# Kernel tuning notes

Measured on AMD Instinct MI355X. Metric: run time of the kernel, lower is better.

## Reference

```python
import jax, jax.numpy as jnp
import numpy as np

N = 50000      # nodes
E = 1000000    # edges
D = 128        # in_dim
H = 4          # heads
C = 32         # hidden_dim (per head)
ED = 16        # edge_input_dim
NEG_SLOPE = 0.2
LN_EPS = 1e-5


def setup_inputs() -> dict:
    key = jax.random.key(0)
    ks = jax.random.split(key, 8)
    w = lambda k, shape: jax.random.normal(k, shape, jnp.float32) * 0.05
    return {
        "x": jax.random.normal(ks[0], (N, D), jnp.float32),
        "edge_index": jax.random.randint(ks[1], (2, E), 0, N, jnp.int32),
        "edge_attr": jax.random.normal(ks[2], (E, ED), jnp.float32),
        "Wl": w(ks[3], (D, H * C)),          # lin_l weight (source transform)
        "bl": jnp.zeros((H * C,), jnp.float32),
        "Wr": w(ks[4], (D, H * C)),          # lin_r weight (target transform)
        "br": jnp.zeros((H * C,), jnp.float32),
        "We": w(ks[5], (ED, H * C)),         # lin_edge weight (no bias in PyG)
        "att": w(ks[6], (H, C)),             # attention vector a per head
        "bias_out": jnp.zeros((H * C,), jnp.float32),  # conv output bias
        "gamma": jnp.ones((H * C,), jnp.float32),      # LayerNorm weight
        "beta": jnp.zeros((H * C,), jnp.float32),      # LayerNorm bias
    }


def _layer_norm(h, gamma, beta):
    mu = jnp.mean(h, axis=-1, keepdims=True)
    var = jnp.mean(jnp.square(h - mu), axis=-1, keepdims=True)
    return (h - mu) * jax.lax.rsqrt(var + LN_EPS) * gamma + beta


def reference(x, edge_index, edge_attr, Wl, bl, Wr, br, We, att, bias_out, gamma, beta):
    src = edge_index[0]
    dst = edge_index[1]

    # GATv2: separate linear transforms for source (lin_l) and target (lin_r)
    x_l = (x @ Wl + bl).reshape(N, H, C)
    x_r = (x @ Wr + br).reshape(N, H, C)
    e = (edge_attr @ We).reshape(E, H, C)

    # per-edge message: leaky_relu(x_l[src] + x_r[dst] + edge), score = <., att>
    m = jax.nn.leaky_relu(x_l[src] + x_r[dst] + e, NEG_SLOPE)   # [E,H,C]
    alpha = jnp.einsum("ehc,hc->eh", m, att)                      # [E,H]

    # segment softmax over incoming edges of each destination node
    amax = jax.ops.segment_max(alpha, dst, num_segments=N)        # [N,H]
    ex = jnp.exp(alpha - amax[dst])
    denom = jax.ops.segment_sum(ex, dst, num_segments=N)          # [N,H]
    attn = ex / (denom[dst] + 1e-16)                              # [E,H]

    # scatter-aggregate weighted source features (x_j = x_l[src] in GATv2)
    out = jax.ops.segment_sum(attn[:, :, None] * x_l[src], dst, num_segments=N)  # [N,H,C]
    out = out.reshape(N, H * C) + bias_out

    h = jax.nn.elu(out)          # dropout is identity at inference
    return _layer_norm(h + x, gamma, beta)   # residual is Identity (D == H*C)
```

## Files before the change

### kernel.cpp

```cpp
#include <hip/hip_runtime.h>
#include <math.h>

#define NN 50000
#define EE 1000000

#define LINB 782
#define CNT_THREADS (EE / 4)
#define CNTB ((CNT_THREADS + 255) / 256)

typedef float f32x4 __attribute__((ext_vector_type(4)));
typedef __bf16 bf16x8 __attribute__((ext_vector_type(8)));

__global__ __launch_bounds__(256) void lin_count_kernel(
    const float* __restrict__ x,
    const float* __restrict__ Wl, const float* __restrict__ bl,
    const float* __restrict__ Wr, const float* __restrict__ br,
    float* __restrict__ xl, float* __restrict__ xr,
    const int* __restrict__ dst, int* __restrict__ counts, int* __restrict__ rank)
{
  const int tid = threadIdx.x;

  if (blockIdx.x >= LINB) {
    int t = (blockIdx.x - LINB) * 256 + tid;
    if (t < CNT_THREADS) {
      int4 d4 = ((const int4*)dst)[t];
      int4 r4;
      r4.x = atomicAdd(&counts[d4.x], 1);
      r4.y = atomicAdd(&counts[d4.y], 1);
      r4.z = atomicAdd(&counts[d4.z], 1);
      r4.w = atomicAdd(&counts[d4.w], 1);
      ((int4*)rank)[t] = r4;
    }
    return;
  }

  __shared__ __bf16 wt[256 * 128];

  {
    #pragma unroll
    for (int half = 0; half < 2; ++half) {
      const float* __restrict__ Wsrc = half ? Wr : Wl;
      const int cbase = half * 128;
      for (int it = 0; it < 16; ++it) {
        int g  = it * 256 + tid;
        int k  = g >> 5;
        int c4 = (g & 31) * 4;
        float4 v = ((const float4*)Wsrc)[g];
        #pragma unroll
        for (int j = 0; j < 4; ++j) {
          int c = cbase + c4 + j;
          int byte = c * 256 + k * 2;
          byte ^= ((c & 7) << 4);
          float f = (j == 0) ? v.x : (j == 1) ? v.y : (j == 2) ? v.z : v.w;
          *(__bf16*)((char*)wt + byte) = (__bf16)f;
        }
      }
    }
  }
  __syncthreads();

  const int wave = tid >> 6;
  const int lane = tid & 63;
  const int l15  = lane & 15;
  const int lhi  = lane >> 4;

  const int row_a   = blockIdx.x * 64 + wave * 16 + l15;
  const int row_a_c = row_a < NN ? row_a : NN - 1;

  f32x4 acc[16];
  #pragma unroll
  for (int t = 0; t < 16; ++t) acc[t] = (f32x4)0.f;

  #pragma unroll
  for (int kk = 0; kk < 4; ++kk) {
    const float* ap = x + (size_t)row_a_c * 128 + kk * 32 + lhi * 8;
    float4 a0 = *(const float4*)ap;
    float4 a1 = *(const float4*)(ap + 4);
    bf16x8 af;
    af[0] = (__bf16)a0.x; af[1] = (__bf16)a0.y; af[2] = (__bf16)a0.z; af[3] = (__bf16)a0.w;
    af[4] = (__bf16)a1.x; af[5] = (__bf16)a1.y; af[6] = (__bf16)a1.z; af[7] = (__bf16)a1.w;
    #pragma unroll
    for (int nt = 0; nt < 16; ++nt) {
      int col  = nt * 16 + l15;
      int byte = col * 256 + (kk * 32 + lhi * 8) * 2;
      byte ^= ((col & 7) << 4);
      bf16x8 bf = *(const bf16x8*)((const char*)wt + byte);
      acc[nt] = __builtin_amdgcn_mfma_f32_16x16x32_bf16(af, bf, acc[nt], 0, 0, 0);
    }
  }

  const int row_base = blockIdx.x * 64 + wave * 16 + lhi * 4;
  #pragma unroll
  for (int nt = 0; nt < 16; ++nt) {
    int col = nt * 16 + l15;
    float bv = (col < 128) ? bl[col] : br[col - 128];
    float* dp = (col < 128) ? (xl + col) : (xr + (col - 128));
    #pragma unroll
    for (int j = 0; j < 4; ++j) {
      int r = row_base + j;
      if (r < NN) dp[(size_t)r * 128] = acc[nt][j] + bv;
    }
  }
}

__global__ __launch_bounds__(1024) void scan_kernel(const int* __restrict__ counts,
                                                    int* __restrict__ row_ptr)
{
  __shared__ int s[1024];
  const int t = threadIdx.x;
  const int CH = (NN + 1023) / 1024;
  const int base = t * CH;
  int sum = 0;
  for (int j = 0; j < CH; ++j) {
    int idx = base + j;
    if (idx < NN) sum += counts[idx];
  }
  s[t] = sum;
  __syncthreads();
  for (int ofs = 1; ofs < 1024; ofs <<= 1) {
    int v = (t >= ofs) ? s[t - ofs] : 0;
    __syncthreads();
    s[t] += v;
    __syncthreads();
  }
  int run = s[t] - sum;
  for (int j = 0; j < CH; ++j) {
    int idx = base + j;
    if (idx < NN) { row_ptr[idx] = run; run += counts[idx]; }
  }
  if (t == 1023) row_ptr[NN] = s[1023];
}

__global__ __launch_bounds__(256) void fill_kernel(const int* __restrict__ src,
                                                   const int* __restrict__ dst,
                                                   const int* __restrict__ rank,
                                                   const int* __restrict__ row_ptr,
                                                   int2* __restrict__ csr)
{
  int t = blockIdx.x * 256 + threadIdx.x;
  if (t >= CNT_THREADS) return;
  int4 s4 = ((const int4*)src)[t];
  int4 d4 = ((const int4*)dst)[t];
  int4 r4 = ((const int4*)rank)[t];
  int e0 = t * 4;
  csr[row_ptr[d4.x] + r4.x] = make_int2(s4.x, e0 + 0);
  csr[row_ptr[d4.y] + r4.y] = make_int2(s4.y, e0 + 1);
  csr[row_ptr[d4.z] + r4.z] = make_int2(s4.z, e0 + 2);
  csr[row_ptr[d4.w] + r4.w] = make_int2(s4.w, e0 + 3);
}

template<int CTRL>
__device__ __forceinline__ float dpp_add(float v)
{
  int y = __builtin_amdgcn_update_dpp(0, __float_as_int(v), CTRL, 0xF, 0xF, true);
  return v + __int_as_float(y);
}

__device__ __forceinline__ float head_reduce32(float v)
{
  v = dpp_add<0xB1>(v);
  v = dpp_add<0x4E>(v);
  v = dpp_add<0x141>(v);
  v = dpp_add<0x140>(v);
  int y = __builtin_amdgcn_ds_swizzle(__float_as_int(v), 0x401F);
  return v + __int_as_float(y);
}

__device__ __forceinline__ void edge_compute(
    float v0, float v1, float4 e0, float4 e1, float4 e2, float4 e3,
    float4 Wa0, float4 Wa1, float4 Wa2, float4 Wa3,
    float4 Wb0, float4 Wb1, float4 Wb2, float4 Wb3,
    float att0, float att1, float xr0, float xr1,
    float& S0, float& S1, float& A0, float& A1)
{
  float s0 = xr0, s1 = xr1;
  s0 = fmaf(e0.x, Wa0.x, s0); s1 = fmaf(e0.x, Wb0.x, s1);
  s0 = fmaf(e0.y, Wa0.y, s0); s1 = fmaf(e0.y, Wb0.y, s1);
  s0 = fmaf(e0.z, Wa0.z, s0); s1 = fmaf(e0.z, Wb0.z, s1);
  s0 = fmaf(e0.w, Wa0.w, s0); s1 = fmaf(e0.w, Wb0.w, s1);
  s0 = fmaf(e1.x, Wa1.x, s0); s1 = fmaf(e1.x, Wb1.x, s1);
  s0 = fmaf(e1.y, Wa1.y, s0); s1 = fmaf(e1.y, Wb1.y, s1);
  s0 = fmaf(e1.z, Wa1.z, s0); s1 = fmaf(e1.z, Wb1.z, s1);
  s0 = fmaf(e1.w, Wa1.w, s0); s1 = fmaf(e1.w, Wb1.w, s1);
  s0 = fmaf(e2.x, Wa2.x, s0); s1 = fmaf(e2.x, Wb2.x, s1);
  s0 = fmaf(e2.y, Wa2.y, s0); s1 = fmaf(e2.y, Wb2.y, s1);
  s0 = fmaf(e2.z, Wa2.z, s0); s1 = fmaf(e2.z, Wb2.z, s1);
  s0 = fmaf(e2.w, Wa2.w, s0); s1 = fmaf(e2.w, Wb2.w, s1);
  s0 = fmaf(e3.x, Wa3.x, s0); s1 = fmaf(e3.x, Wb3.x, s1);
  s0 = fmaf(e3.y, Wa3.y, s0); s1 = fmaf(e3.y, Wb3.y, s1);
  s0 = fmaf(e3.z, Wa3.z, s0); s1 = fmaf(e3.z, Wb3.z, s1);
  s0 = fmaf(e3.w, Wa3.w, s0); s1 = fmaf(e3.w, Wb3.w, s1);

  float u0 = v0 + s0;
  float u1 = v1 + s1;
  u0 = fmaxf(u0, 0.2f * u0);
  u1 = fmaxf(u1, 0.2f * u1);

  float t0 = head_reduce32(u0 * att0);
  float t1 = head_reduce32(u1 * att1);

  float p0 = __expf(t0);
  float p1 = __expf(t1);
  S0 += p0;  S1 += p1;
  A0 = fmaf(p0, v0, A0);
  A1 = fmaf(p1, v1, A1);
}

__global__ __launch_bounds__(256, 2) void node_kernel(
    const float* __restrict__ x,
    const float* __restrict__ edge_attr,
    const float* __restrict__ We,
    const float* __restrict__ att,
    const float* __restrict__ bias_out,
    const float* __restrict__ gamma,
    const float* __restrict__ beta,
    const float* __restrict__ xl,
    const float* __restrict__ xr,
    const int* __restrict__ row_ptr,
    const int2* __restrict__ csr,
    float* __restrict__ out)
{
  const int lane = threadIdx.x & 63;
  const int n = blockIdx.x * 4 + (threadIdx.x >> 6);
  const int c0 = lane;
  const int c1 = lane + 64;

  float4 Wa0 = make_float4(We[ 0*128+c0], We[ 1*128+c0], We[ 2*128+c0], We[ 3*128+c0]);
  float4 Wa1 = make_float4(We[ 4*128+c0], We[ 5*128+c0], We[ 6*128+c0], We[ 7*128+c0]);
  float4 Wa2 = make_float4(We[ 8*128+c0], We[ 9*128+c0], We[10*128+c0], We[11*128+c0]);
  float4 Wa3 = make_float4(We[12*128+c0], We[13*128+c0], We[14*128+c0], We[15*128+c0]);
  float4 Wb0 = make_float4(We[ 0*128+c1], We[ 1*128+c1], We[ 2*128+c1], We[ 3*128+c1]);
  float4 Wb1 = make_float4(We[ 4*128+c1], We[ 5*128+c1], We[ 6*128+c1], We[ 7*128+c1]);
  float4 Wb2 = make_float4(We[ 8*128+c1], We[ 9*128+c1], We[10*128+c1], We[11*128+c1]);
  float4 Wb3 = make_float4(We[12*128+c1], We[13*128+c1], We[14*128+c1], We[15*128+c1]);

  const float att0 = att[c0], att1 = att[c1];
  const float xr0 = xr[(size_t)n * 128 + c0];
  const float xr1 = xr[(size_t)n * 128 + c1];

  const int i0 = __builtin_amdgcn_readfirstlane(row_ptr[n]);
  const int i1 = __builtin_amdgcn_readfirstlane(row_ptr[n + 1]);

  float S0a = 0.f, S1a = 0.f, A0a = 0.f, A1a = 0.f;
  float S0b = 0.f, S1b = 0.f, A0b = 0.f, A1b = 0.f;

  int i = i0;
  for (; i + 1 < i1; i += 2) {
    int2 sea = csr[i];
    int2 seb = csr[i + 1];
    int sa  = __builtin_amdgcn_readfirstlane(sea.x);
    int eia = __builtin_amdgcn_readfirstlane(sea.y);
    int sb  = __builtin_amdgcn_readfirstlane(seb.x);
    int eib = __builtin_amdgcn_readfirstlane(seb.y);

    const float* xla = xl + (size_t)sa * 128;
    const float* xlb = xl + (size_t)sb * 128;
    float va0 = xla[c0], va1 = xla[c1];
    float vb0 = xlb[c0], vb1 = xlb[c1];

    const float4* eaa = (const float4*)(edge_attr + (size_t)eia * 16);
    const float4* eab = (const float4*)(edge_attr + (size_t)eib * 16);
    float4 a0 = eaa[0], a1 = eaa[1], a2 = eaa[2], a3 = eaa[3];
    float4 b0 = eab[0], b1 = eab[1], b2 = eab[2], b3 = eab[3];

    edge_compute(va0, va1, a0, a1, a2, a3,
                 Wa0, Wa1, Wa2, Wa3, Wb0, Wb1, Wb2, Wb3,
                 att0, att1, xr0, xr1, S0a, S1a, A0a, A1a);
    edge_compute(vb0, vb1, b0, b1, b2, b3,
                 Wa0, Wa1, Wa2, Wa3, Wb0, Wb1, Wb2, Wb3,
                 att0, att1, xr0, xr1, S0b, S1b, A0b, A1b);
  }
  if (i < i1) {
    int2 se = csr[i];
    int s   = __builtin_amdgcn_readfirstlane(se.x);
    int eid = __builtin_amdgcn_readfirstlane(se.y);
    const float* xlp = xl + (size_t)s * 128;
    float v0 = xlp[c0], v1 = xlp[c1];
    const float4* ea4 = (const float4*)(edge_attr + (size_t)eid * 16);
    float4 a0 = ea4[0], a1 = ea4[1], a2 = ea4[2], a3 = ea4[3];
    edge_compute(v0, v1, a0, a1, a2, a3,
                 Wa0, Wa1, Wa2, Wa3, Wb0, Wb1, Wb2, Wb3,
                 att0, att1, xr0, xr1, S0a, S1a, A0a, A1a);
  }

  float S0 = S0a + S0b, S1 = S1a + S1b;
  float A0 = A0a + A0b, A1 = A1a + A1b;

  float o0 = A0 / (S0 + 1e-16f) + bias_out[c0];
  float o1 = A1 / (S1 + 1e-16f) + bias_out[c1];
  float h0 = o0 > 0.f ? o0 : expm1f(o0);
  float h1 = o1 > 0.f ? o1 : expm1f(o1);
  float r0 = h0 + x[(size_t)n * 128 + c0];
  float r1 = h1 + x[(size_t)n * 128 + c1];

  float s1 = r0 + r1;
  float s2 = r0 * r0 + r1 * r1;
  #pragma unroll
  for (int m = 1; m < 64; m <<= 1) {
    s1 += __shfl_xor(s1, m, 64);
    s2 += __shfl_xor(s2, m, 64);
  }
  float mean = s1 * (1.f / 128.f);
  float var  = s2 * (1.f / 128.f) - mean * mean;
  float rstd = rsqrtf(var + 1e-5f);
  out[(size_t)n * 128 + c0] = (r0 - mean) * rstd * gamma[c0] + beta[c0];
  out[(size_t)n * 128 + c1] = (r1 - mean) * rstd * gamma[c1] + beta[c1];
}

extern "C" void kernel_launch(void* const* d_in, const int* in_sizes, int n_in,
                              void* d_out, int out_size, void* d_ws, size_t ws_size,
                              hipStream_t stream)
{
  const float* x         = (const float*)d_in[0];
  const int*   edge_idx  = (const int*)d_in[1];
  const float* edge_attr = (const float*)d_in[2];
  const float* Wl        = (const float*)d_in[3];
  const float* bl        = (const float*)d_in[4];
  const float* Wr        = (const float*)d_in[5];
  const float* br        = (const float*)d_in[6];
  const float* We        = (const float*)d_in[7];
  const float* att       = (const float*)d_in[8];
  const float* bias_out  = (const float*)d_in[9];
  const float* gamma     = (const float*)d_in[10];
  const float* beta      = (const float*)d_in[11];
  float* out = (float*)d_out;

  const int* src = edge_idx;
  const int* dst = edge_idx + EE;

  char* ws = (char*)d_ws;
  float* xl = (float*)ws;            ws += (size_t)NN * 128 * 4;
  float* xr = (float*)ws;            ws += (size_t)NN * 128 * 4;
  int* counts  = (int*)ws;           ws += (size_t)NN * 4;
  int* rank    = (int*)ws;           ws += (size_t)EE * 4;
  int* row_ptr = (int*)ws;           ws += (size_t)(NN + 16) * 4;
  int2* csr = (int2*)ws;

  hipMemsetAsync(counts, 0, (size_t)NN * 4, stream);

  lin_count_kernel<<<LINB + CNTB, 256, 0, stream>>>(
      x, Wl, bl, Wr, br, xl, xr, dst, counts, rank);
  scan_kernel<<<1, 1024, 0, stream>>>(counts, row_ptr);
  fill_kernel<<<CNTB, 256, 0, stream>>>(src, dst, rank, row_ptr, csr);
  node_kernel<<<NN / 4, 256, 0, stream>>>(x, edge_attr, We, att, bias_out, gamma, beta,
                                          xl, xr, row_ptr, csr, out);
}
```

Baseline: 436.4 us.

## Pre-swizzle bf16 weight image once and unroll node edge loop by four

A new single-block prep kernel converts Wl/Wr to a swizzled bf16 image once, so each of the 782 linear blocks fills its LDS tile with direct global-to-LDS loads instead of converting fp32 weights with scattered 2-byte shared stores. The node kernel's edge loop is unrolled from two to four independent edges with four accumulator sets, giving more gathers in flight to hide latency. The cost is an extra kernel launch, more registers in the node kernel and a different summation order.

```diff
diff --git a/kernel.cpp b/kernel.cpp
--- a/kernel.cpp
+++ b/kernel.cpp
@@ -11,10 +11,28 @@
 typedef float f32x4 __attribute__((ext_vector_type(4)));
 typedef __bf16 bf16x8 __attribute__((ext_vector_type(8)));
 
+typedef __attribute__((address_space(1))) const void gvoid_t;
+typedef __attribute__((address_space(3))) void svoid_t;
+
+__global__ __launch_bounds__(256) void prep_kernel(
+    const float* __restrict__ Wl, const float* __restrict__ Wr, __bf16* __restrict__ img)
+{
+  const int c  = threadIdx.x;
+  const int cc = c & 127;
+  const float* __restrict__ Wsrc = (c < 128) ? Wl : Wr;
+  for (int k0 = 0; k0 < 128; k0 += 8) {
+    bf16x8 v;
+    #pragma unroll
+    for (int j = 0; j < 8; ++j) v[j] = (__bf16)Wsrc[(size_t)(k0 + j) * 128 + cc];
+    int byte = (c * 256 + k0 * 2) ^ ((c & 7) << 4);
+    *(bf16x8*)((char*)img + byte) = v;
+  }
+}
+
 __global__ __launch_bounds__(256) void lin_count_kernel(
     const float* __restrict__ x,
-    const float* __restrict__ Wl, const float* __restrict__ bl,
-    const float* __restrict__ Wr, const float* __restrict__ br,
+    const __bf16* __restrict__ img,
+    const float* __restrict__ bl, const float* __restrict__ br,
     float* __restrict__ xl, float* __restrict__ xr,
     const int* __restrict__ dst, int* __restrict__ counts, int* __restrict__ rank)
 {
@@ -37,24 +55,13 @@
   __shared__ __bf16 wt[256 * 128];
 
   {
+    const int wv = tid >> 6, ln = tid & 63;
     #pragma unroll
-    for (int half = 0; half < 2; ++half) {
-      const float* __restrict__ Wsrc = half ? Wr : Wl;
-      const int cbase = half * 128;
-      for (int it = 0; it < 16; ++it) {
-        int g  = it * 256 + tid;
-        int k  = g >> 5;
-        int c4 = (g & 31) * 4;
-        float4 v = ((const float4*)Wsrc)[g];
-        #pragma unroll
-        for (int j = 0; j < 4; ++j) {
-          int c = cbase + c4 + j;
-          int byte = c * 256 + k * 2;
-          byte ^= ((c & 7) << 4);
-          float f = (j == 0) ? v.x : (j == 1) ? v.y : (j == 2) ? v.z : v.w;
-          *(__bf16*)((char*)wt + byte) = (__bf16)f;
-        }
-      }
+    for (int it = 0; it < 16; ++it) {
+      int off = wv * 16384 + it * 1024;
+      __builtin_amdgcn_global_load_lds(
+          (gvoid_t*)((const char*)img + off + ln * 16),
+          (svoid_t*)((char*)wt + off), 16, 0, 0);
     }
   }
   __syncthreads();
@@ -82,8 +89,7 @@
     #pragma unroll
     for (int nt = 0; nt < 16; ++nt) {
       int col  = nt * 16 + l15;
-      int byte = col * 256 + (kk * 32 + lhi * 8) * 2;
-      byte ^= ((col & 7) << 4);
+      int byte = (col * 256 + (kk * 32 + lhi * 8) * 2) ^ ((col & 7) << 4);
       bf16x8 bf = *(const bf16x8*)((const char*)wt + byte);
       acc[nt] = __builtin_amdgcn_mfma_f32_16x16x32_bf16(af, bf, acc[nt], 0, 0, 0);
     }
@@ -241,36 +247,52 @@
   const int i0 = __builtin_amdgcn_readfirstlane(row_ptr[n]);
   const int i1 = __builtin_amdgcn_readfirstlane(row_ptr[n + 1]);
 
-  float S0a = 0.f, S1a = 0.f, A0a = 0.f, A1a = 0.f;
-  float S0b = 0.f, S1b = 0.f, A0b = 0.f, A1b = 0.f;
+  float Sa0 = 0.f, Sa1 = 0.f, Aa0 = 0.f, Aa1 = 0.f;
+  float Sb0 = 0.f, Sb1 = 0.f, Ab0 = 0.f, Ab1 = 0.f;
+  float Sc0 = 0.f, Sc1 = 0.f, Ac0 = 0.f, Ac1 = 0.f;
+  float Sd0 = 0.f, Sd1 = 0.f, Ad0 = 0.f, Ad1 = 0.f;
 
   int i = i0;
-  for (; i + 1 < i1; i += 2) {
-    int2 sea = csr[i];
-    int2 seb = csr[i + 1];
-    int sa  = __builtin_amdgcn_readfirstlane(sea.x);
-    int eia = __builtin_amdgcn_readfirstlane(sea.y);
-    int sb  = __builtin_amdgcn_readfirstlane(seb.x);
-    int eib = __builtin_amdgcn_readfirstlane(seb.y);
-
-    const float* xla = xl + (size_t)sa * 128;
-    const float* xlb = xl + (size_t)sb * 128;
-    float va0 = xla[c0], va1 = xla[c1];
-    float vb0 = xlb[c0], vb1 = xlb[c1];
-
-    const float4* eaa = (const float4*)(edge_attr + (size_t)eia * 16);
-    const float4* eab = (const float4*)(edge_attr + (size_t)eib * 16);
-    float4 a0 = eaa[0], a1 = eaa[1], a2 = eaa[2], a3 = eaa[3];
-    float4 b0 = eab[0], b1 = eab[1], b2 = eab[2], b3 = eab[3];
-
-    edge_compute(va0, va1, a0, a1, a2, a3,
-                 Wa0, Wa1, Wa2, Wa3, Wb0, Wb1, Wb2, Wb3,
-                 att0, att1, xr0, xr1, S0a, S1a, A0a, A1a);
-    edge_compute(vb0, vb1, b0, b1, b2, b3,
-                 Wa0, Wa1, Wa2, Wa3, Wb0, Wb1, Wb2, Wb3,
-                 att0, att1, xr0, xr1, S0b, S1b, A0b, A1b);
-  }
-  if (i < i1) {
+  for (; i + 3 < i1; i += 4) {
+    int2 se0 = csr[i],     se1 = csr[i + 1];
+    int2 se2 = csr[i + 2], se3 = csr[i + 3];
+    int s0i = __builtin_amdgcn_readfirstlane(se0.x);
+    int e0i = __builtin_amdgcn_readfirstlane(se0.y);
+    int s1i = __builtin_amdgcn_readfirstlane(se1.x);
+    int e1i = __builtin_amdgcn_readfirstlane(se1.y);
+    int s2i = __builtin_amdgcn_readfirstlane(se2.x);
+    int e2i = __builtin_amdgcn_readfirstlane(se2.y);
+    int s3i = __builtin_amdgcn_readfirstlane(se3.x);
+    int e3i = __builtin_amdgcn_readfirstlane(se3.y);
+
+    const float* p0 = xl + (size_t)s0i * 128;
+    const float* p1 = xl + (size_t)s1i * 128;
+    const float* p2 = xl + (size_t)s2i * 128;
+    const float* p3 = xl + (size_t)s3i * 128;
+    float v00 = p0[c0], v01 = p0[c1];
+    float v10 = p1[c0], v11 = p1[c1];
+    float v20 = p2[c0], v21 = p2[c1];
+    float v30 = p3[c0], v31 = p3[c1];
+
+    const float4* q0 = (const float4*)(edge_attr + (size_t)e0i * 16);
+    const float4* q1 = (const float4*)(edge_attr + (size_t)e1i * 16);
+    const float4* q2 = (const float4*)(edge_attr + (size_t)e2i * 16);
+    const float4* q3 = (const float4*)(edge_attr + (size_t)e3i * 16);
+    float4 a00 = q0[0], a01 = q0[1], a02 = q0[2], a03 = q0[3];
+    float4 a10 = q1[0], a11 = q1[1], a12 = q1[2], a13 = q1[3];
+    float4 a20 = q2[0], a21 = q2[1], a22 = q2[2], a23 = q2[3];
+    float4 a30 = q3[0], a31 = q3[1], a32 = q3[2], a33 = q3[3];
+
+    edge_compute(v00, v01, a00, a01, a02, a03, Wa0, Wa1, Wa2, Wa3, Wb0, Wb1, Wb2, Wb3,
+                 att0, att1, xr0, xr1, Sa0, Sa1, Aa0, Aa1);
+    edge_compute(v10, v11, a10, a11, a12, a13, Wa0, Wa1, Wa2, Wa3, Wb0, Wb1, Wb2, Wb3,
+                 att0, att1, xr0, xr1, Sb0, Sb1, Ab0, Ab1);
+    edge_compute(v20, v21, a20, a21, a22, a23, Wa0, Wa1, Wa2, Wa3, Wb0, Wb1, Wb2, Wb3,
+                 att0, att1, xr0, xr1, Sc0, Sc1, Ac0, Ac1);
+    edge_compute(v30, v31, a30, a31, a32, a33, Wa0, Wa1, Wa2, Wa3, Wb0, Wb1, Wb2, Wb3,
+                 att0, att1, xr0, xr1, Sd0, Sd1, Ad0, Ad1);
+  }
+  for (; i < i1; ++i) {
     int2 se = csr[i];
     int s   = __builtin_amdgcn_readfirstlane(se.x);
     int eid = __builtin_amdgcn_readfirstlane(se.y);
@@ -278,13 +300,14 @@
     float v0 = xlp[c0], v1 = xlp[c1];
     const float4* ea4 = (const float4*)(edge_attr + (size_t)eid * 16);
     float4 a0 = ea4[0], a1 = ea4[1], a2 = ea4[2], a3 = ea4[3];
-    edge_compute(v0, v1, a0, a1, a2, a3,
-                 Wa0, Wa1, Wa2, Wa3, Wb0, Wb1, Wb2, Wb3,
-                 att0, att1, xr0, xr1, S0a, S1a, A0a, A1a);
-  }
-
-  float S0 = S0a + S0b, S1 = S1a + S1b;
-  float A0 = A0a + A0b, A1 = A1a + A1b;
+    edge_compute(v0, v1, a0, a1, a2, a3, Wa0, Wa1, Wa2, Wa3, Wb0, Wb1, Wb2, Wb3,
+                 att0, att1, xr0, xr1, Sa0, Sa1, Aa0, Aa1);
+  }
+
+  float S0 = (Sa0 + Sb0) + (Sc0 + Sd0);
+  float S1 = (Sa1 + Sb1) + (Sc1 + Sd1);
+  float A0 = (Aa0 + Ab0) + (Ac0 + Ad0);
+  float A1 = (Aa1 + Ab1) + (Ac1 + Ad1);
 
   float o0 = A0 / (S0 + 1e-16f) + bias_out[c0];
   float o1 = A1 / (S1 + 1e-16f) + bias_out[c1];
@@ -334,12 +357,14 @@
   int* counts  = (int*)ws;           ws += (size_t)NN * 4;
   int* rank    = (int*)ws;           ws += (size_t)EE * 4;
   int* row_ptr = (int*)ws;           ws += (size_t)(NN + 16) * 4;
-  int2* csr = (int2*)ws;
+  int2* csr = (int2*)ws;             ws += (size_t)EE * 8;
+  __bf16* img = (__bf16*)ws;
 
   hipMemsetAsync(counts, 0, (size_t)NN * 4, stream);
 
+  prep_kernel<<<1, 256, 0, stream>>>(Wl, Wr, img);
   lin_count_kernel<<<LINB + CNTB, 256, 0, stream>>>(
-      x, Wl, bl, Wr, br, xl, xr, dst, counts, rank);
+      x, img, bl, br, xl, xr, dst, counts, rank);
   scan_kernel<<<1, 1024, 0, stream>>>(counts, row_ptr);
   fill_kernel<<<CNTB, 256, 0, stream>>>(src, dst, rank, row_ptr, csr);
   node_kernel<<<NN / 4, 256, 0, stream>>>(x, edge_attr, We, att, bias_out, gamma, beta,
```

New measurement: 448.2 us. +2.7%, slower.

## Pre-swizzle bf16 weight image once and load it to LDS asynchronously

Applied to the files above, without the earlier changes.

The Wl/Wr fp32→bf16 conversion and swizzle is moved out of each of the 782 GEMM blocks into one extra block of the counting kernel, which writes a global bf16 image. The GEMM blocks then copy that image straight into LDS with global_load_lds. The GEMM is also moved to run alongside the CSR fill instead of the atomic count, changing which work overlaps. This removes redundant per-block conversion. The cost is an extra global buffer and a serial dependency on the single weight-prep block inside the count kernel.

```diff
diff --git a/kernel.cpp b/kernel.cpp
--- a/kernel.cpp
+++ b/kernel.cpp
@@ -11,25 +11,91 @@
 typedef float f32x4 __attribute__((ext_vector_type(4)));
 typedef __bf16 bf16x8 __attribute__((ext_vector_type(8)));
 
-__global__ __launch_bounds__(256) void lin_count_kernel(
+typedef __attribute__((address_space(1))) const void gvoid_t;
+typedef __attribute__((address_space(3))) void svoid_t;
+
+__global__ __launch_bounds__(256) void prep_count_kernel(
+    const float* __restrict__ Wl, const float* __restrict__ Wr, __bf16* __restrict__ img,
+    const int* __restrict__ dst, int* __restrict__ counts, int* __restrict__ rank)
+{
+  const int tid = threadIdx.x;
+
+  if (blockIdx.x == 0) {
+    const int c  = tid;
+    const int cc = c & 127;
+    const float* __restrict__ Wsrc = (c < 128) ? Wl : Wr;
+    for (int k0 = 0; k0 < 128; k0 += 8) {
+      bf16x8 v;
+      #pragma unroll
+      for (int j = 0; j < 8; ++j) v[j] = (__bf16)Wsrc[(size_t)(k0 + j) * 128 + cc];
+      int byte = (c * 256 + k0 * 2) ^ ((c & 7) << 4);
+      *(bf16x8*)((char*)img + byte) = v;
+    }
+    return;
+  }
+
+  int t = (blockIdx.x - 1) * 256 + tid;
+  if (t < CNT_THREADS) {
+    int4 d4 = ((const int4*)dst)[t];
+    int4 r4;
+    r4.x = atomicAdd(&counts[d4.x], 1);
+    r4.y = atomicAdd(&counts[d4.y], 1);
+    r4.z = atomicAdd(&counts[d4.z], 1);
+    r4.w = atomicAdd(&counts[d4.w], 1);
+    ((int4*)rank)[t] = r4;
+  }
+}
+
+__global__ __launch_bounds__(1024) void scan_kernel(const int* __restrict__ counts,
+                                                    int* __restrict__ row_ptr)
+{
+  __shared__ int s[1024];
+  const int t = threadIdx.x;
+  const int CH = (NN + 1023) / 1024;
+  const int base = t * CH;
+  int sum = 0;
+  for (int j = 0; j < CH; ++j) {
+    int idx = base + j;
+    if (idx < NN) sum += counts[idx];
+  }
+  s[t] = sum;
+  __syncthreads();
+  for (int ofs = 1; ofs < 1024; ofs <<= 1) {
+    int v = (t >= ofs) ? s[t - ofs] : 0;
+    __syncthreads();
+    s[t] += v;
+    __syncthreads();
+  }
+  int run = s[t] - sum;
+  for (int j = 0; j < CH; ++j) {
+    int idx = base + j;
+    if (idx < NN) { row_ptr[idx] = run; run += counts[idx]; }
+  }
+  if (t == 1023) row_ptr[NN] = s[1023];
+}
+
+__global__ __launch_bounds__(256) void lin_fill_kernel(
     const float* __restrict__ x,
-    const float* __restrict__ Wl, const float* __restrict__ bl,
-    const float* __restrict__ Wr, const float* __restrict__ br,
+    const __bf16* __restrict__ img,
+    const float* __restrict__ bl, const float* __restrict__ br,
     float* __restrict__ xl, float* __restrict__ xr,
-    const int* __restrict__ dst, int* __restrict__ counts, int* __restrict__ rank)
+    const int* __restrict__ src, const int* __restrict__ dst,
+    const int* __restrict__ rank, const int* __restrict__ row_ptr,
+    int2* __restrict__ csr)
 {
   const int tid = threadIdx.x;
 
   if (blockIdx.x >= LINB) {
     int t = (blockIdx.x - LINB) * 256 + tid;
     if (t < CNT_THREADS) {
+      int4 s4 = ((const int4*)src)[t];
       int4 d4 = ((const int4*)dst)[t];
-      int4 r4;
-      r4.x = atomicAdd(&counts[d4.x], 1);
-      r4.y = atomicAdd(&counts[d4.y], 1);
-      r4.z = atomicAdd(&counts[d4.z], 1);
-      r4.w = atomicAdd(&counts[d4.w], 1);
-      ((int4*)rank)[t] = r4;
+      int4 r4 = ((const int4*)rank)[t];
+      int e0 = t * 4;
+      csr[row_ptr[d4.x] + r4.x] = make_int2(s4.x, e0 + 0);
+      csr[row_ptr[d4.y] + r4.y] = make_int2(s4.y, e0 + 1);
+      csr[row_ptr[d4.z] + r4.z] = make_int2(s4.z, e0 + 2);
+      csr[row_ptr[d4.w] + r4.w] = make_int2(s4.w, e0 + 3);
     }
     return;
   }
@@ -37,24 +103,13 @@
   __shared__ __bf16 wt[256 * 128];
 
   {
+    const int wv = tid >> 6, ln = tid & 63;
     #pragma unroll
-    for (int half = 0; half < 2; ++half) {
-      const float* __restrict__ Wsrc = half ? Wr : Wl;
-      const int cbase = half * 128;
-      for (int it = 0; it < 16; ++it) {
-        int g  = it * 256 + tid;
-        int k  = g >> 5;
-        int c4 = (g & 31) * 4;
-        float4 v = ((const float4*)Wsrc)[g];
-        #pragma unroll
-        for (int j = 0; j < 4; ++j) {
-          int c = cbase + c4 + j;
-          int byte = c * 256 + k * 2;
-          byte ^= ((c & 7) << 4);
-          float f = (j == 0) ? v.x : (j == 1) ? v.y : (j == 2) ? v.z : v.w;
-          *(__bf16*)((char*)wt + byte) = (__bf16)f;
-        }
-      }
+    for (int it = 0; it < 16; ++it) {
+      int off = wv * 16384 + it * 1024;
+      __builtin_amdgcn_global_load_lds(
+          (gvoid_t*)((const char*)img + off + ln * 16),
+          (svoid_t*)((char*)wt + off), 16, 0, 0);
     }
   }
   __syncthreads();
@@ -82,8 +137,7 @@
     #pragma unroll
     for (int nt = 0; nt < 16; ++nt) {
       int col  = nt * 16 + l15;
-      int byte = col * 256 + (kk * 32 + lhi * 8) * 2;
-      byte ^= ((col & 7) << 4);
+      int byte = (col * 256 + (kk * 32 + lhi * 8) * 2) ^ ((col & 7) << 4);
       bf16x8 bf = *(const bf16x8*)((const char*)wt + byte);
       acc[nt] = __builtin_amdgcn_mfma_f32_16x16x32_bf16(af, bf, acc[nt], 0, 0, 0);
     }
@@ -101,52 +155,6 @@
       if (r < NN) dp[(size_t)r * 128] = acc[nt][j] + bv;
     }
   }
-}
-
-__global__ __launch_bounds__(1024) void scan_kernel(const int* __restrict__ counts,
-                                                    int* __restrict__ row_ptr)
-{
-  __shared__ int s[1024];
-  const int t = threadIdx.x;
-  const int CH = (NN + 1023) / 1024;
-  const int base = t * CH;
-  int sum = 0;
-  for (int j = 0; j < CH; ++j) {
-    int idx = base + j;
-    if (idx < NN) sum += counts[idx];
-  }
-  s[t] = sum;
-  __syncthreads();
-  for (int ofs = 1; ofs < 1024; ofs <<= 1) {
-    int v = (t >= ofs) ? s[t - ofs] : 0;
-    __syncthreads();
-    s[t] += v;
-    __syncthreads();
-  }
-  int run = s[t] - sum;
-  for (int j = 0; j < CH; ++j) {
-    int idx = base + j;
-    if (idx < NN) { row_ptr[idx] = run; run += counts[idx]; }
-  }
-  if (t == 1023) row_ptr[NN] = s[1023];
-}
-
-__global__ __launch_bounds__(256) void fill_kernel(const int* __restrict__ src,
-                                                   const int* __restrict__ dst,
-                                                   const int* __restrict__ rank,
-                                                   const int* __restrict__ row_ptr,
-                                                   int2* __restrict__ csr)
-{
-  int t = blockIdx.x * 256 + threadIdx.x;
-  if (t >= CNT_THREADS) return;
-  int4 s4 = ((const int4*)src)[t];
-  int4 d4 = ((const int4*)dst)[t];
-  int4 r4 = ((const int4*)rank)[t];
-  int e0 = t * 4;
-  csr[row_ptr[d4.x] + r4.x] = make_int2(s4.x, e0 + 0);
-  csr[row_ptr[d4.y] + r4.y] = make_int2(s4.y, e0 + 1);
-  csr[row_ptr[d4.z] + r4.z] = make_int2(s4.z, e0 + 2);
-  csr[row_ptr[d4.w] + r4.w] = make_int2(s4.w, e0 + 3);
 }
 
 template<int CTRL>
@@ -334,14 +342,15 @@
   int* counts  = (int*)ws;           ws += (size_t)NN * 4;
   int* rank    = (int*)ws;           ws += (size_t)EE * 4;
   int* row_ptr = (int*)ws;           ws += (size_t)(NN + 16) * 4;
-  int2* csr = (int2*)ws;
+  int2* csr = (int2*)ws;             ws += (size_t)EE * 8;
+  __bf16* img = (__bf16*)ws;
 
   hipMemsetAsync(counts, 0, (size_t)NN * 4, stream);
 
-  lin_count_kernel<<<LINB + CNTB, 256, 0, stream>>>(
-      x, Wl, bl, Wr, br, xl, xr, dst, counts, rank);
+  prep_count_kernel<<<CNTB + 1, 256, 0, stream>>>(Wl, Wr, img, dst, counts, rank);
   scan_kernel<<<1, 1024, 0, stream>>>(counts, row_ptr);
-  fill_kernel<<<CNTB, 256, 0, stream>>>(src, dst, rank, row_ptr, csr);
+  lin_fill_kernel<<<LINB + CNTB, 256, 0, stream>>>(
+      x, img, bl, br, xl, xr, src, dst, rank, row_ptr, csr);
   node_kernel<<<NN / 4, 256, 0, stream>>>(x, edge_attr, We, att, bias_out, gamma, beta,
                                           xl, xr, row_ptr, csr, out);
 }
```

Measured after the change: 427.5 us. -2.0%, faster.
